# Performance work log

Measured on AMD Instinct MI355X. Metric: run time of the kernel, lower is better.

The kernel has to match this reference:

```python
import jax, jax.numpy as jnp
import numpy as np

N_NODES = 20000
N_EDGES = 320000
IN_C = 256
HID = 32
HEADS0 = 4  # n_heads[0]: both #modules in first layer and heads per module
OUT_C = 40
NEG_SLOPE = 0.2


def _segment_softmax(e, seg, n):
    # e: [E, H], softmax over edges grouped by destination node
    m = jax.ops.segment_max(e, seg, num_segments=n)
    m = jnp.where(jnp.isfinite(m), m, 0.0)  # nodes with no in-edges
    ex = jnp.exp(e - m[seg])
    s = jax.ops.segment_sum(ex, seg, num_segments=n)
    return ex / (s[seg] + 1e-16)


def _gat_conv(x, W, a_src, a_dst, bias, src, dst, n, concat):
    # PyG GATConv math (self-loops assumed already appended to src/dst)
    H, C = a_src.shape
    h = (x @ W).reshape(n, H, C)                      # [N, H, C]
    e_src = (h * a_src).sum(-1)                       # [N, H]
    e_dst = (h * a_dst).sum(-1)                       # [N, H]
    e = jax.nn.leaky_relu(e_src[src] + e_dst[dst], NEG_SLOPE)  # [E, H]
    alpha = _segment_softmax(e, dst, n)               # [E, H]
    out = jax.ops.segment_sum(h[src] * alpha[:, :, None], dst, num_segments=n)
    if concat:
        return out.reshape(n, H * C) + bias
    return out.mean(axis=1) + bias


def setup_inputs() -> dict:
    key = jax.random.key(0)
    ks = jax.random.split(key, 12)
    x = jax.random.normal(ks[0], (N_NODES, IN_C), dtype=jnp.float32)
    edge_index = jax.random.randint(ks[1], (2, N_EDGES), 0, N_NODES, dtype=jnp.int32)
    M = HEADS0  # number of first-layer modules
    W1 = jax.random.normal(ks[2], (M, IN_C, HEADS0 * HID), dtype=jnp.float32) * 0.1
    a_src1 = jax.random.normal(ks[3], (M, HEADS0, HID), dtype=jnp.float32) * 0.1
    a_dst1 = jax.random.normal(ks[4], (M, HEADS0, HID), dtype=jnp.float32) * 0.1
    b1 = jax.random.normal(ks[5], (M, HEADS0 * HID), dtype=jnp.float32) * 0.1
    cat_dim = M * HEADS0 * HID  # 512: actual width after torch.cat over modules
    W2 = jax.random.normal(ks[6], (cat_dim, OUT_C), dtype=jnp.float32) * 0.1
    a_src2 = jax.random.normal(ks[7], (1, OUT_C), dtype=jnp.float32) * 0.1
    a_dst2 = jax.random.normal(ks[8], (1, OUT_C), dtype=jnp.float32) * 0.1
    b2 = jax.random.normal(ks[9], (OUT_C,), dtype=jnp.float32) * 0.1
    return {"x": x, "edge_index": edge_index, "W1": W1, "a_src1": a_src1,
            "a_dst1": a_dst1, "b1": b1, "W2": W2, "a_src2": a_src2,
            "a_dst2": a_dst2, "b2": b2}


def reference(x, edge_index, W1, a_src1, a_dst1, b1, W2, a_src2, a_dst2, b2):
    n = x.shape[0]
    loops = jnp.arange(n, dtype=edge_index.dtype)  # PyG add_self_loops=True
    src = jnp.concatenate([edge_index[0], loops])
    dst = jnp.concatenate([edge_index[1], loops])
    # first layer: HEADS0 independent GATConv modules, outputs concatenated
    outs = jax.vmap(lambda W, a_s, a_d, b: _gat_conv(x, W, a_s, a_d, b, src, dst, n, True))(
        W1, a_src1, a_dst1, b1)                      # [M, N, HEADS0*HID]
    h = jnp.transpose(outs, (1, 0, 2)).reshape(n, -1)  # [N, 512]
    h = jax.nn.elu(h)  # dropout is a no-op in eval mode
    out = _gat_conv(h, W2, a_src2, a_dst2, b2, src, dst, n, False)  # [N, OUT_C]
    return jax.nn.log_softmax(out, axis=1)
```

## Files before the change

### kernel.cpp

```cpp
#include <hip/hip_runtime.h>
#include <cstdint>
#include <cstddef>

#define N_NODES 20000
#define N_EDGES 320000
#define E_TOT   340000
#define IN_C    256
#define HID     32
#define HEADS0  4
#define OUT_C   40
#define NEG_SLOPE 0.2f
#define CAT     512
#define MH      16
#define H2S     48

typedef unsigned short ushort_t;
typedef __attribute__((ext_vector_type(8))) short short8v;
typedef __attribute__((ext_vector_type(4))) float f32x4;
typedef __attribute__((ext_vector_type(8))) unsigned short ushort8v;

#define WAVE_FENCE() asm volatile("" ::: "memory")

__device__ inline float bf2f(unsigned short u) {
  union { unsigned int i; float f; } c; c.i = ((unsigned int)u) << 16; return c.f;
}
__device__ inline unsigned short f2bf(float f) {
  union { float f; unsigned int i; } c; c.f = f;
  unsigned int r = c.i + 0x7FFFu + ((c.i >> 16) & 1u);
  return (unsigned short)(r >> 16);
}


__global__ __launch_bounds__(256) void degree_k(const int* __restrict__ ei, int* __restrict__ deg) {
  int e = blockIdx.x * 256 + threadIdx.x;
  if (e >= E_TOT) return;
  int d = (e < N_EDGES) ? ei[N_EDGES + e] : (e - N_EDGES);
  atomicAdd(&deg[d], 1);
}

__global__ __launch_bounds__(1024) void scan_k(const int* __restrict__ deg, int* __restrict__ row_ptr) {
  const int C = 20;
  __shared__ int part[1024];
  int t = threadIdx.x;
  int b = t * C;
  int s = 0;
  for (int i = 0; i < C; i++) { int idx = b + i; if (idx < N_NODES) s += deg[idx]; }
  part[t] = s;
  __syncthreads();
  for (int off = 1; off < 1024; off <<= 1) {
    int v = part[t];
    int u = (t >= off) ? part[t - off] : 0;
    __syncthreads();
    part[t] = v + u;
    __syncthreads();
  }
  int run = (t > 0) ? part[t - 1] : 0;
  for (int i = 0; i < C; i++) {
    int idx = b + i;
    if (idx <= N_NODES) {
      row_ptr[idx] = run;
      if (idx < N_NODES) run += deg[idx];
    }
  }
}

__global__ __launch_bounds__(256) void scatter_score_k(const int* __restrict__ ei,
                                                       const int* __restrict__ row_ptr,
                                                       int* __restrict__ fill,
                                                       int* __restrict__ csr_src,
                                                       const float* __restrict__ es1,
                                                       const float* __restrict__ ed1,
                                                       ushort_t* __restrict__ exq) {
  int e = blockIdx.x * 256 + threadIdx.x;
  if (e >= E_TOT) return;
  int s, d;
  if (e < N_EDGES) { s = ei[e]; d = ei[N_EDGES + e]; }
  else             { s = e - N_EDGES; d = s; }
  int pos = row_ptr[d] + atomicAdd(&fill[d], 1);
  csr_src[pos] = s;

  const float4* sp = (const float4*)(es1 + (size_t)s * MH);
  const float4* dp = (const float4*)(ed1 + (size_t)d * MH);
  float4 a0 = sp[0], a1 = sp[1], a2 = sp[2], a3 = sp[3];
  float4 b0 = dp[0], b1 = dp[1], b2 = dp[2], b3 = dp[3];
  float v[16] = {a0.x + b0.x, a0.y + b0.y, a0.z + b0.z, a0.w + b0.w,
                 a1.x + b1.x, a1.y + b1.y, a1.z + b1.z, a1.w + b1.w,
                 a2.x + b2.x, a2.y + b2.y, a2.z + b2.z, a2.w + b2.w,
                 a3.x + b3.x, a3.y + b3.y, a3.z + b3.z, a3.w + b3.w};
  ushort8v o0, o1;
#pragma unroll
  for (int i = 0; i < 16; i++) {
    float ev = v[i];
    ev = (ev > 0.f) ? ev : ev * NEG_SLOPE;
    float ex = __expf(ev);
    if (i < 8) o0[i] = f2bf(ex); else o1[i - 8] = f2bf(ex);
  }
  *(ushort8v*)(exq + (size_t)pos * MH)     = o0;
  *(ushort8v*)(exq + (size_t)pos * MH + 8) = o1;
}

#define XB (N_NODES * IN_C / 4 / 256)

__global__ __launch_bounds__(256) void prep_k(const float* __restrict__ x,
                                              ushort_t* __restrict__ xhi,
                                              ushort_t* __restrict__ xlo,
                                              const float* __restrict__ W1,
                                              ushort_t* __restrict__ bhi,
                                              ushort_t* __restrict__ blo,
                                              const float* __restrict__ W2,
                                              ushort_t* __restrict__ b2hi,
                                              ushort_t* __restrict__ b2lo) {
  int blk = blockIdx.x;
  if (blk < XB) {
    int i = blk * 256 + threadIdx.x;
    float4 v = ((const float4*)x)[i];
    ushort_t hi[4], lo[4];
    float vv[4] = {v.x, v.y, v.z, v.w};
#pragma unroll
    for (int k = 0; k < 4; k++) {
      ushort_t h = f2bf(vv[k]);
      hi[k] = h;
      lo[k] = f2bf(vv[k] - bf2f(h));
    }
    ((ushort4*)xhi)[i] = make_ushort4(hi[0], hi[1], hi[2], hi[3]);
    ((ushort4*)xlo)[i] = make_ushort4(lo[0], lo[1], lo[2], lo[3]);
  } else if (blk < XB + 64) {
    int idx = (blk - XB) * 256 + threadIdx.x;
    int n16  = idx >> 9;
    int k32  = (idx >> 6) & 7;
    int lane = idx & 63;
    int cfull = n16 * 16 + (lane & 15);
    int m = cfull >> 7;
    int c = cfull & 127;
    int kbase = k32 * 32 + (lane >> 4) * 8;
#pragma unroll
    for (int b = 0; b < 8; b++) {
      float v = W1[((m << 8) + kbase + b) * 128 + c];
      ushort_t h = f2bf(v);
      bhi[(size_t)idx * 8 + b] = h;
      blo[(size_t)idx * 8 + b] = f2bf(v - bf2f(h));
    }
  } else {
    int idx = (blk - XB - 64) * 256 + threadIdx.x;
    int n16  = idx >> 10;
    int k32  = (idx >> 6) & 15;
    int lane = idx & 63;
    int n = n16 * 16 + (lane & 15);
    int kbase = k32 * 32 + (lane >> 4) * 8;
#pragma unroll
    for (int b = 0; b < 8; b++) {
      float v = (n < OUT_C) ? W2[(kbase + b) * OUT_C + n] : 0.f;
      ushort_t h = f2bf(v);
      b2hi[(size_t)idx * 8 + b] = h;
      b2lo[(size_t)idx * 8 + b] = f2bf(v - bf2f(h));
    }
  }
}

__global__ __launch_bounds__(256) void gemm1_mfma_k(const ushort_t* __restrict__ xhi,
                                                    const ushort_t* __restrict__ xlo,
                                                    const ushort_t* __restrict__ bhi,
                                                    const ushort_t* __restrict__ blo,
                                                    const float* __restrict__ a_src1,
                                                    const float* __restrict__ a_dst1,
                                                    ushort_t* __restrict__ h1b,
                                                    float* __restrict__ es1,
                                                    float* __restrict__ ed1) {
  int tid = threadIdx.x;
  int wave = tid >> 6, lane = tid & 63;
  int l15 = lane & 15, lhi = lane >> 4;
  int wrow = blockIdx.x * 64 + (wave & 1) * 32;
  int wcol = blockIdx.y * 128 + (wave >> 1) * 64;
  int n16base = wcol >> 4;

  f32x4 acc[2][4];
#pragma unroll
  for (int mf = 0; mf < 2; mf++)
#pragma unroll
    for (int nf = 0; nf < 4; nf++) acc[mf][nf] = (f32x4){0.f, 0.f, 0.f, 0.f};

  int arow[2];
#pragma unroll
  for (int mf = 0; mf < 2; mf++) {
    int r = wrow + mf * 16 + l15;
    arow[mf] = (r < N_NODES) ? r : (N_NODES - 1);
  }

  for (int ks = 0; ks < 8; ks++) {
    short8v ah[2], al[2];
#pragma unroll
    for (int mf = 0; mf < 2; mf++) {
      size_t off = (size_t)arow[mf] * IN_C + ks * 32 + lhi * 8;
      ah[mf] = *(const short8v*)(xhi + off);
      al[mf] = *(const short8v*)(xlo + off);
    }
    short8v bh[4], bl[4];
#pragma unroll
    for (int nf = 0; nf < 4; nf++) {
      size_t off = ((size_t)((n16base + nf) * 8 + ks) * 64 + lane) * 8;
      bh[nf] = *(const short8v*)(bhi + off);
      bl[nf] = *(const short8v*)(blo + off);
    }
#pragma unroll
    for (int mf = 0; mf < 2; mf++)
#pragma unroll
      for (int nf = 0; nf < 4; nf++) {
        acc[mf][nf] = __builtin_amdgcn_mfma_f32_16x16x32_bf16(ah[mf], bh[nf], acc[mf][nf], 0, 0, 0);
        acc[mf][nf] = __builtin_amdgcn_mfma_f32_16x16x32_bf16(ah[mf], bl[nf], acc[mf][nf], 0, 0, 0);
        acc[mf][nf] = __builtin_amdgcn_mfma_f32_16x16x32_bf16(al[mf], bh[nf], acc[mf][nf], 0, 0, 0);
      }
  }

#pragma unroll
  for (int mf = 0; mf < 2; mf++) {
    int rbase = wrow + mf * 16 + lhi * 4;
#pragma unroll
    for (int nf = 0; nf < 4; nf++) {
      int col = wcol + nf * 16 + l15;
#pragma unroll
      for (int r = 0; r < 4; r++) {
        int row = rbase + r;
        if (row < N_NODES)
          h1b[(size_t)row * CAT + col] = f2bf(acc[mf][nf][r]);
      }
    }
  }

  int mh0 = wcol >> 5;
  float as[4], ad[4];
#pragma unroll
  for (int nf = 0; nf < 4; nf++) {
    int aidx = (mh0 + (nf >> 1)) * HID + (nf & 1) * 16 + l15;
    as[nf] = a_src1[aidx];
    ad[nf] = a_dst1[aidx];
  }
#pragma unroll
  for (int mf = 0; mf < 2; mf++) {
#pragma unroll
    for (int r = 0; r < 4; r++) {
      int row = wrow + mf * 16 + lhi * 4 + r;
      float ps0 = acc[mf][0][r] * as[0] + acc[mf][1][r] * as[1];
      float ps1 = acc[mf][2][r] * as[2] + acc[mf][3][r] * as[3];
      float pd0 = acc[mf][0][r] * ad[0] + acc[mf][1][r] * ad[1];
      float pd1 = acc[mf][2][r] * ad[2] + acc[mf][3][r] * ad[3];
#pragma unroll
      for (int msk = 1; msk < 16; msk <<= 1) {
        ps0 += __shfl_xor(ps0, msk); ps1 += __shfl_xor(ps1, msk);
        pd0 += __shfl_xor(pd0, msk); pd1 += __shfl_xor(pd1, msk);
      }
      if (l15 == 0 && row < N_NODES) {
        es1[row * MH + mh0]     = ps0;
        es1[row * MH + mh0 + 1] = ps1;
        ed1[row * MH + mh0]     = pd0;
        ed1[row * MH + mh0 + 1] = pd1;
      }
    }
  }
}


__global__ __launch_bounds__(256) void agg1_k(const ushort_t* __restrict__ h1b,
                                              const ushort_t* __restrict__ exq,
                                              const int* __restrict__ row_ptr,
                                              const int* __restrict__ csr_src,
                                              const float* __restrict__ b1,
                                              ushort_t* __restrict__ hhi,
                                              ushort_t* __restrict__ hlo) {
  int w = threadIdx.x >> 6, lane = threadIdx.x & 63;
  int n = blockIdx.x * 4 + w;
  int beg = row_ptr[n];
  int deg = row_ptr[n + 1] - beg;
  int hh = lane >> 2;

  __shared__ float ex_buf[4][64][MH + 1];
  __shared__ int   src_buf[4][64];

  float s_part[MH];
#pragma unroll
  for (int i = 0; i < MH; i++) s_part[i] = 0.f;
  float acc[8];
#pragma unroll
  for (int j = 0; j < 8; j++) acc[j] = 0.f;

  for (int base = 0; base < deg; base += 64) {
    int cnt = min(64, deg - base);
    if (lane < cnt) {
      int p = beg + base + lane;
      src_buf[w][lane] = csr_src[p];
      ushort8v q0 = *(const ushort8v*)(exq + (size_t)p * MH);
      ushort8v q1 = *(const ushort8v*)(exq + (size_t)p * MH + 8);
#pragma unroll
      for (int i = 0; i < 8; i++) {
        float ex = bf2f(q0[i]);
        ex_buf[w][lane][i] = ex;
        s_part[i] += ex;
      }
#pragma unroll
      for (int i = 0; i < 8; i++) {
        float ex = bf2f(q1[i]);
        ex_buf[w][lane][8 + i] = ex;
        s_part[8 + i] += ex;
      }
    }
    WAVE_FENCE();
    int e = 0;
    for (; e + 3 < cnt; e += 4) {
      int s0 = src_buf[w][e + 0], s1 = src_buf[w][e + 1];
      int s2 = src_buf[w][e + 2], s3 = src_buf[w][e + 3];
      float x0 = ex_buf[w][e + 0][hh], x1 = ex_buf[w][e + 1][hh];
      float x2 = ex_buf[w][e + 2][hh], x3 = ex_buf[w][e + 3][hh];
      ushort8v v0 = *(const ushort8v*)(h1b + (size_t)s0 * CAT + lane * 8);
      ushort8v v1 = *(const ushort8v*)(h1b + (size_t)s1 * CAT + lane * 8);
      ushort8v v2 = *(const ushort8v*)(h1b + (size_t)s2 * CAT + lane * 8);
      ushort8v v3 = *(const ushort8v*)(h1b + (size_t)s3 * CAT + lane * 8);
#pragma unroll
      for (int j = 0; j < 8; j++) acc[j] += x0 * bf2f(v0[j]);
#pragma unroll
      for (int j = 0; j < 8; j++) acc[j] += x1 * bf2f(v1[j]);
#pragma unroll
      for (int j = 0; j < 8; j++) acc[j] += x2 * bf2f(v2[j]);
#pragma unroll
      for (int j = 0; j < 8; j++) acc[j] += x3 * bf2f(v3[j]);
    }
    for (; e < cnt; e++) {
      int s = src_buf[w][e];
      float xv = ex_buf[w][e][hh];
      ushort8v hv = *(const ushort8v*)(h1b + (size_t)s * CAT + lane * 8);
#pragma unroll
      for (int j = 0; j < 8; j++) acc[j] += xv * bf2f(hv[j]);
    }
    WAVE_FENCE();
  }

  float denom = 0.f;
#pragma unroll
  for (int i = 0; i < MH; i++) {
    float v = s_part[i];
    v += __shfl_xor(v, 1);  v += __shfl_xor(v, 2);  v += __shfl_xor(v, 4);
    v += __shfl_xor(v, 8);  v += __shfl_xor(v, 16); v += __shfl_xor(v, 32);
    if (hh == i) denom = v;
  }
  denom += 1e-16f;

  const float4* b1p = (const float4*)(b1 + lane * 8);
  float4 bq0 = b1p[0], bq1 = b1p[1];
  float bv8[8] = {bq0.x, bq0.y, bq0.z, bq0.w, bq1.x, bq1.y, bq1.z, bq1.w};

  ushort8v vhi, vlo;
#pragma unroll
  for (int j = 0; j < 8; j++) {
    float o = acc[j] / denom + bv8[j];
    float e = (o > 0.f) ? o : (__expf(o) - 1.f);
    ushort_t h = f2bf(e);
    vhi[j] = h;
    vlo[j] = f2bf(e - bf2f(h));
  }
  *(ushort8v*)(hhi + (size_t)n * CAT + lane * 8) = vhi;
  *(ushort8v*)(hlo + (size_t)n * CAT + lane * 8) = vlo;
}

__global__ __launch_bounds__(256) void gemm2_mfma_k(const ushort_t* __restrict__ hhi,
                                                    const ushort_t* __restrict__ hlo,
                                                    const ushort_t* __restrict__ b2hi,
                                                    const ushort_t* __restrict__ b2lo,
                                                    const float* __restrict__ a_src2,
                                                    const float* __restrict__ a_dst2,
                                                    ushort_t* __restrict__ h2b,
                                                    float* __restrict__ es2,
                                                    float* __restrict__ ed2) {
  int tid = threadIdx.x;
  int wave = tid >> 6, lane = tid & 63;
  int l15 = lane & 15, lhi = lane >> 4;
  int wrow = blockIdx.x * 64 + wave * 16;

  f32x4 acc[3];
#pragma unroll
  for (int nf = 0; nf < 3; nf++) acc[nf] = (f32x4){0.f, 0.f, 0.f, 0.f};

  int r0 = wrow + l15;
  int arow = (r0 < N_NODES) ? r0 : (N_NODES - 1);

  for (int ks = 0; ks < 16; ks++) {
    size_t aoff = (size_t)arow * CAT + ks * 32 + lhi * 8;
    short8v ah = *(const short8v*)(hhi + aoff);
    short8v al = *(const short8v*)(hlo + aoff);
#pragma unroll
    for (int nf = 0; nf < 3; nf++) {
      size_t boff = ((size_t)(nf * 16 + ks) * 64 + lane) * 8;
      short8v bh = *(const short8v*)(b2hi + boff);
      short8v bl = *(const short8v*)(b2lo + boff);
      acc[nf] = __builtin_amdgcn_mfma_f32_16x16x32_bf16(ah, bh, acc[nf], 0, 0, 0);
      acc[nf] = __builtin_amdgcn_mfma_f32_16x16x32_bf16(ah, bl, acc[nf], 0, 0, 0);
      acc[nf] = __builtin_amdgcn_mfma_f32_16x16x32_bf16(al, bh, acc[nf], 0, 0, 0);
    }
  }

  float av[3], bv[3];
#pragma unroll
  for (int nf = 0; nf < 3; nf++) {
    int col = nf * 16 + l15;
    av[nf] = (col < OUT_C) ? a_src2[col] : 0.f;
    bv[nf] = (col < OUT_C) ? a_dst2[col] : 0.f;
  }
#pragma unroll
  for (int r = 0; r < 4; r++) {
    int row = wrow + lhi * 4 + r;
    float ps = acc[0][r] * av[0] + acc[1][r] * av[1] + acc[2][r] * av[2];
    float pd = acc[0][r] * bv[0] + acc[1][r] * bv[1] + acc[2][r] * bv[2];
    ps += __shfl_xor(ps, 1); pd += __shfl_xor(pd, 1);
    ps += __shfl_xor(ps, 2); pd += __shfl_xor(pd, 2);
    ps += __shfl_xor(ps, 4); pd += __shfl_xor(pd, 4);
    ps += __shfl_xor(ps, 8); pd += __shfl_xor(pd, 8);
    if (row < N_NODES) {
#pragma unroll
      for (int nf = 0; nf < 3; nf++)
        h2b[(size_t)row * H2S + nf * 16 + l15] = f2bf(acc[nf][r]);
      if (l15 == 0) { es2[row] = ps; ed2[row] = pd; }
    }
  }
}

__global__ __launch_bounds__(256) void agg2_k(const ushort_t* __restrict__ h2b,
                                              const float* __restrict__ es2,
                                              const float* __restrict__ ed2,
                                              const int* __restrict__ row_ptr,
                                              const int* __restrict__ csr_src,
                                              const float* __restrict__ b2,
                                              float* __restrict__ out) {
  int w = threadIdx.x >> 6, lane = threadIdx.x & 63;
  int n = blockIdx.x * 4 + w;
  int beg = row_ptr[n];
  int deg = row_ptr[n + 1] - beg;
  float edn = ed2[n];

  __shared__ float exb[4][64];
  __shared__ int   srb[4][64];

  float acc = 0.f, ssum = 0.f;
  for (int base = 0; base < deg; base += 64) {
    int cnt = min(64, deg - base);
    if (lane < cnt) {
      int s = csr_src[beg + base + lane];
      srb[w][lane] = s;
      float ev = es2[s] + edn;
      ev = (ev > 0.f) ? ev : ev * NEG_SLOPE;
      float ex = __expf(ev);
      exb[w][lane] = ex;
      ssum += ex;
    }
    WAVE_FENCE();
    int e = 0;
    for (; e + 3 < cnt; e += 4) {
      int s0 = srb[w][e], s1 = srb[w][e + 1], s2 = srb[w][e + 2], s3 = srb[w][e + 3];
      float x0 = exb[w][e], x1 = exb[w][e + 1], x2 = exb[w][e + 2], x3 = exb[w][e + 3];
      if (lane < OUT_C) {
        float v0 = bf2f(h2b[(size_t)s0 * H2S + lane]);
        float v1 = bf2f(h2b[(size_t)s1 * H2S + lane]);
        float v2 = bf2f(h2b[(size_t)s2 * H2S + lane]);
        float v3 = bf2f(h2b[(size_t)s3 * H2S + lane]);
        acc += x0 * v0; acc += x1 * v1; acc += x2 * v2; acc += x3 * v3;
      }
    }
    for (; e < cnt; e++) {
      int s = srb[w][e];
      float xv = exb[w][e];
      if (lane < OUT_C) acc += xv * bf2f(h2b[(size_t)s * H2S + lane]);
    }
    WAVE_FENCE();
  }

  ssum += __shfl_xor(ssum, 1); ssum += __shfl_xor(ssum, 2); ssum += __shfl_xor(ssum, 4);
  ssum += __shfl_xor(ssum, 8); ssum += __shfl_xor(ssum, 16); ssum += __shfl_xor(ssum, 32);

  float val = (lane < OUT_C) ? (acc / (ssum + 1e-16f) + b2[lane]) : -INFINITY;

  float rmax = val;
#pragma unroll
  for (int o = 1; o < 64; o <<= 1) rmax = fmaxf(rmax, __shfl_xor(rmax, o));
  float ex = (lane < OUT_C) ? __expf(val - rmax) : 0.f;
  float sume = ex;
#pragma unroll
  for (int o = 1; o < 64; o <<= 1) sume += __shfl_xor(sume, o);
  if (lane < OUT_C) out[(size_t)n * OUT_C + lane] = val - rmax - __logf(sume);
}


extern "C" void kernel_launch(void* const* d_in, const int* in_sizes, int n_in,
                              void* d_out, int out_size, void* d_ws, size_t ws_size,
                              hipStream_t stream) {
  const float* x      = (const float*)d_in[0];
  const int*   ei     = (const int*)d_in[1];
  const float* W1     = (const float*)d_in[2];
  const float* a_src1 = (const float*)d_in[3];
  const float* a_dst1 = (const float*)d_in[4];
  const float* b1     = (const float*)d_in[5];
  const float* W2     = (const float*)d_in[6];
  const float* a_src2 = (const float*)d_in[7];
  const float* a_dst2 = (const float*)d_in[8];
  const float* b2     = (const float*)d_in[9];
  float* out = (float*)d_out;

  char* ws = (char*)d_ws;
  size_t off = 0;
  auto alloc = [&](size_t bytes) -> void* {
    void* p = ws + off;
    off += (bytes + 255) & ~(size_t)255;
    return p;
  };
  ushort_t* xhi  = (ushort_t*)alloc((size_t)N_NODES * IN_C * 2);
  ushort_t* xlo  = (ushort_t*)alloc((size_t)N_NODES * IN_C * 2);
  ushort_t* bhi  = (ushort_t*)alloc((size_t)32 * 8 * 64 * 8 * 2);
  ushort_t* blo  = (ushort_t*)alloc((size_t)32 * 8 * 64 * 8 * 2);
  ushort_t* b2hi = (ushort_t*)alloc((size_t)3 * 16 * 64 * 8 * 2);
  ushort_t* b2lo = (ushort_t*)alloc((size_t)3 * 16 * 64 * 8 * 2);
  ushort_t* h1b  = (ushort_t*)alloc((size_t)N_NODES * CAT * 2);
  ushort_t* hhi  = (ushort_t*)alloc((size_t)N_NODES * CAT * 2);
  ushort_t* hlo  = (ushort_t*)alloc((size_t)N_NODES * CAT * 2);
  float* es1     = (float*)alloc((size_t)N_NODES * MH * 4);
  float* ed1     = (float*)alloc((size_t)N_NODES * MH * 4);
  ushort_t* h2b  = (ushort_t*)alloc((size_t)N_NODES * H2S * 2);
  float* es2     = (float*)alloc((size_t)N_NODES * 4);
  float* ed2     = (float*)alloc((size_t)N_NODES * 4);
  int*   deg     = (int*)alloc((size_t)N_NODES * 4);
  int*   fill    = (int*)alloc((size_t)N_NODES * 4);
  int*   row_ptr = (int*)alloc((size_t)(N_NODES + 1) * 4);
  int*   csr_src = (int*)alloc((size_t)E_TOT * 4);
  ushort_t* exq  = xhi;

  hipMemsetAsync(deg, 0, ((size_t)N_NODES * 4 + 255 & ~(size_t)255) + (size_t)N_NODES * 4, stream);

  degree_k<<<(E_TOT + 255) / 256, 256, 0, stream>>>(ei, deg);
  scan_k<<<1, 1024, 0, stream>>>(deg, row_ptr);
  prep_k<<<XB + 64 + 12, 256, 0, stream>>>(x, xhi, xlo, W1, bhi, blo, W2, b2hi, b2lo);
  gemm1_mfma_k<<<dim3((N_NODES + 63) / 64, CAT / 128), 256, 0, stream>>>(
      xhi, xlo, bhi, blo, a_src1, a_dst1, h1b, es1, ed1);
  scatter_score_k<<<(E_TOT + 255) / 256, 256, 0, stream>>>(
      ei, row_ptr, fill, csr_src, es1, ed1, exq);
  agg1_k<<<N_NODES / 4, 256, 0, stream>>>(h1b, exq, row_ptr, csr_src, b1, hhi, hlo);
  gemm2_mfma_k<<<(N_NODES + 63) / 64, 256, 0, stream>>>(hhi, hlo, b2hi, b2lo, a_src2, a_dst2, h2b, es2, ed2);
  agg2_k<<<N_NODES / 4, 256, 0, stream>>>(h2b, es2, ed2, row_ptr, csr_src, b2, out);
}
```

Measured before the change: 207.8 us.

## Split x to bf16 hi/lo inside gemm1, fold degree count into prep, drop lo term in gemm2

```diff
diff --git a/kernel.cpp b/kernel.cpp
--- a/kernel.cpp
+++ b/kernel.cpp
@@ -30,12 +30,54 @@
   return (unsigned short)(r >> 16);
 }
 
-
-__global__ __launch_bounds__(256) void degree_k(const int* __restrict__ ei, int* __restrict__ deg) {
-  int e = blockIdx.x * 256 + threadIdx.x;
-  if (e >= E_TOT) return;
-  int d = (e < N_EDGES) ? ei[N_EDGES + e] : (e - N_EDGES);
-  atomicAdd(&deg[d], 1);
+#define DEGB ((E_TOT + 255) / 256)
+
+__global__ __launch_bounds__(256) void prep_k(const float* __restrict__ W1,
+                                              ushort_t* __restrict__ bhi,
+                                              ushort_t* __restrict__ blo,
+                                              const float* __restrict__ W2,
+                                              ushort_t* __restrict__ b2hi,
+                                              ushort_t* __restrict__ b2lo,
+                                              const int* __restrict__ ei,
+                                              int* __restrict__ deg) {
+  int blk = blockIdx.x;
+  if (blk < 64) {
+    int idx = blk * 256 + threadIdx.x;
+    int n16  = idx >> 9;
+    int k32  = (idx >> 6) & 7;
+    int lane = idx & 63;
+    int cfull = n16 * 16 + (lane & 15);
+    int m = cfull >> 7;
+    int c = cfull & 127;
+    int kbase = k32 * 32 + (lane >> 4) * 8;
+#pragma unroll
+    for (int b = 0; b < 8; b++) {
+      float v = W1[((m << 8) + kbase + b) * 128 + c];
+      ushort_t h = f2bf(v);
+      bhi[(size_t)idx * 8 + b] = h;
+      blo[(size_t)idx * 8 + b] = f2bf(v - bf2f(h));
+    }
+  } else if (blk < 76) {
+    int idx = (blk - 64) * 256 + threadIdx.x;
+    int n16  = idx >> 10;
+    int k32  = (idx >> 6) & 15;
+    int lane = idx & 63;
+    int n = n16 * 16 + (lane & 15);
+    int kbase = k32 * 32 + (lane >> 4) * 8;
+#pragma unroll
+    for (int b = 0; b < 8; b++) {
+      float v = (n < OUT_C) ? W2[(kbase + b) * OUT_C + n] : 0.f;
+      ushort_t h = f2bf(v);
+      b2hi[(size_t)idx * 8 + b] = h;
+      b2lo[(size_t)idx * 8 + b] = f2bf(v - bf2f(h));
+    }
+  } else {
+    int e = (blk - 76) * 256 + threadIdx.x;
+    if (e < E_TOT) {
+      int d = (e < N_EDGES) ? ei[N_EDGES + e] : (e - N_EDGES);
+      atomicAdd(&deg[d], 1);
+    }
+  }
 }
 
 __global__ __launch_bounds__(1024) void scan_k(const int* __restrict__ deg, int* __restrict__ row_ptr) {
@@ -99,66 +141,7 @@
   *(ushort8v*)(exq + (size_t)pos * MH + 8) = o1;
 }
 
-#define XB (N_NODES * IN_C / 4 / 256)
-
-__global__ __launch_bounds__(256) void prep_k(const float* __restrict__ x,
-                                              ushort_t* __restrict__ xhi,
-                                              ushort_t* __restrict__ xlo,
-                                              const float* __restrict__ W1,
-                                              ushort_t* __restrict__ bhi,
-                                              ushort_t* __restrict__ blo,
-                                              const float* __restrict__ W2,
-                                              ushort_t* __restrict__ b2hi,
-                                              ushort_t* __restrict__ b2lo) {
-  int blk = blockIdx.x;
-  if (blk < XB) {
-    int i = blk * 256 + threadIdx.x;
-    float4 v = ((const float4*)x)[i];
-    ushort_t hi[4], lo[4];
-    float vv[4] = {v.x, v.y, v.z, v.w};
-#pragma unroll
-    for (int k = 0; k < 4; k++) {
-      ushort_t h = f2bf(vv[k]);
-      hi[k] = h;
-      lo[k] = f2bf(vv[k] - bf2f(h));
-    }
-    ((ushort4*)xhi)[i] = make_ushort4(hi[0], hi[1], hi[2], hi[3]);
-    ((ushort4*)xlo)[i] = make_ushort4(lo[0], lo[1], lo[2], lo[3]);
-  } else if (blk < XB + 64) {
-    int idx = (blk - XB) * 256 + threadIdx.x;
-    int n16  = idx >> 9;
-    int k32  = (idx >> 6) & 7;
-    int lane = idx & 63;
-    int cfull = n16 * 16 + (lane & 15);
-    int m = cfull >> 7;
-    int c = cfull & 127;
-    int kbase = k32 * 32 + (lane >> 4) * 8;
-#pragma unroll
-    for (int b = 0; b < 8; b++) {
-      float v = W1[((m << 8) + kbase + b) * 128 + c];
-      ushort_t h = f2bf(v);
-      bhi[(size_t)idx * 8 + b] = h;
-      blo[(size_t)idx * 8 + b] = f2bf(v - bf2f(h));
-    }
-  } else {
-    int idx = (blk - XB - 64) * 256 + threadIdx.x;
-    int n16  = idx >> 10;
-    int k32  = (idx >> 6) & 15;
-    int lane = idx & 63;
-    int n = n16 * 16 + (lane & 15);
-    int kbase = k32 * 32 + (lane >> 4) * 8;
-#pragma unroll
-    for (int b = 0; b < 8; b++) {
-      float v = (n < OUT_C) ? W2[(kbase + b) * OUT_C + n] : 0.f;
-      ushort_t h = f2bf(v);
-      b2hi[(size_t)idx * 8 + b] = h;
-      b2lo[(size_t)idx * 8 + b] = f2bf(v - bf2f(h));
-    }
-  }
-}
-
-__global__ __launch_bounds__(256) void gemm1_mfma_k(const ushort_t* __restrict__ xhi,
-                                                    const ushort_t* __restrict__ xlo,
+__global__ __launch_bounds__(256) void gemm1_mfma_k(const float* __restrict__ x,
                                                     const ushort_t* __restrict__ bhi,
                                                     const ushort_t* __restrict__ blo,
                                                     const float* __restrict__ a_src1,
@@ -190,9 +173,15 @@
     short8v ah[2], al[2];
 #pragma unroll
     for (int mf = 0; mf < 2; mf++) {
-      size_t off = (size_t)arow[mf] * IN_C + ks * 32 + lhi * 8;
-      ah[mf] = *(const short8v*)(xhi + off);
-      al[mf] = *(const short8v*)(xlo + off);
+      const float4* xp = (const float4*)(x + (size_t)arow[mf] * IN_C + ks * 32 + lhi * 8);
+      float4 f0 = xp[0], f1 = xp[1];
+      float av8[8] = {f0.x, f0.y, f0.z, f0.w, f1.x, f1.y, f1.z, f1.w};
+#pragma unroll
+      for (int j = 0; j < 8; j++) {
+        ushort_t h = f2bf(av8[j]);
+        ah[mf][j] = (short)h;
+        al[mf][j] = (short)f2bf(av8[j] - bf2f(h));
+      }
     }
     short8v bh[4], bl[4];
 #pragma unroll
@@ -264,8 +253,7 @@
                                               const int* __restrict__ row_ptr,
                                               const int* __restrict__ csr_src,
                                               const float* __restrict__ b1,
-                                              ushort_t* __restrict__ hhi,
-                                              ushort_t* __restrict__ hlo) {
+                                              ushort_t* __restrict__ h1e) {
   int w = threadIdx.x >> 6, lane = threadIdx.x & 63;
   int n = blockIdx.x * 4 + w;
   int beg = row_ptr[n];
@@ -346,21 +334,17 @@
   float4 bq0 = b1p[0], bq1 = b1p[1];
   float bv8[8] = {bq0.x, bq0.y, bq0.z, bq0.w, bq1.x, bq1.y, bq1.z, bq1.w};
 
-  ushort8v vhi, vlo;
+  ushort8v vhi;
 #pragma unroll
   for (int j = 0; j < 8; j++) {
     float o = acc[j] / denom + bv8[j];
     float e = (o > 0.f) ? o : (__expf(o) - 1.f);
-    ushort_t h = f2bf(e);
-    vhi[j] = h;
-    vlo[j] = f2bf(e - bf2f(h));
-  }
-  *(ushort8v*)(hhi + (size_t)n * CAT + lane * 8) = vhi;
-  *(ushort8v*)(hlo + (size_t)n * CAT + lane * 8) = vlo;
-}
-
-__global__ __launch_bounds__(256) void gemm2_mfma_k(const ushort_t* __restrict__ hhi,
-                                                    const ushort_t* __restrict__ hlo,
+    vhi[j] = f2bf(e);
+  }
+  *(ushort8v*)(h1e + (size_t)n * CAT + lane * 8) = vhi;
+}
+
+__global__ __launch_bounds__(256) void gemm2_mfma_k(const ushort_t* __restrict__ h1e,
                                                     const ushort_t* __restrict__ b2hi,
                                                     const ushort_t* __restrict__ b2lo,
                                                     const float* __restrict__ a_src2,
@@ -382,8 +366,7 @@
 
   for (int ks = 0; ks < 16; ks++) {
     size_t aoff = (size_t)arow * CAT + ks * 32 + lhi * 8;
-    short8v ah = *(const short8v*)(hhi + aoff);
-    short8v al = *(const short8v*)(hlo + aoff);
+    short8v ah = *(const short8v*)(h1e + aoff);
 #pragma unroll
     for (int nf = 0; nf < 3; nf++) {
       size_t boff = ((size_t)(nf * 16 + ks) * 64 + lane) * 8;
@@ -391,7 +374,6 @@
       short8v bl = *(const short8v*)(b2lo + boff);
       acc[nf] = __builtin_amdgcn_mfma_f32_16x16x32_bf16(ah, bh, acc[nf], 0, 0, 0);
       acc[nf] = __builtin_amdgcn_mfma_f32_16x16x32_bf16(ah, bl, acc[nf], 0, 0, 0);
-      acc[nf] = __builtin_amdgcn_mfma_f32_16x16x32_bf16(al, bh, acc[nf], 0, 0, 0);
     }
   }
 
@@ -507,15 +489,13 @@
     off += (bytes + 255) & ~(size_t)255;
     return p;
   };
-  ushort_t* xhi  = (ushort_t*)alloc((size_t)N_NODES * IN_C * 2);
-  ushort_t* xlo  = (ushort_t*)alloc((size_t)N_NODES * IN_C * 2);
   ushort_t* bhi  = (ushort_t*)alloc((size_t)32 * 8 * 64 * 8 * 2);
   ushort_t* blo  = (ushort_t*)alloc((size_t)32 * 8 * 64 * 8 * 2);
   ushort_t* b2hi = (ushort_t*)alloc((size_t)3 * 16 * 64 * 8 * 2);
   ushort_t* b2lo = (ushort_t*)alloc((size_t)3 * 16 * 64 * 8 * 2);
   ushort_t* h1b  = (ushort_t*)alloc((size_t)N_NODES * CAT * 2);
-  ushort_t* hhi  = (ushort_t*)alloc((size_t)N_NODES * CAT * 2);
-  ushort_t* hlo  = (ushort_t*)alloc((size_t)N_NODES * CAT * 2);
+  ushort_t* h1e  = (ushort_t*)alloc((size_t)N_NODES * CAT * 2);
+  ushort_t* exq  = (ushort_t*)alloc((size_t)E_TOT * MH * 2);
   float* es1     = (float*)alloc((size_t)N_NODES * MH * 4);
   float* ed1     = (float*)alloc((size_t)N_NODES * MH * 4);
   ushort_t* h2b  = (ushort_t*)alloc((size_t)N_NODES * H2S * 2);
@@ -525,18 +505,16 @@
   int*   fill    = (int*)alloc((size_t)N_NODES * 4);
   int*   row_ptr = (int*)alloc((size_t)(N_NODES + 1) * 4);
   int*   csr_src = (int*)alloc((size_t)E_TOT * 4);
-  ushort_t* exq  = xhi;
-
-  hipMemsetAsync(deg, 0, ((size_t)N_NODES * 4 + 255 & ~(size_t)255) + (size_t)N_NODES * 4, stream);
-
-  degree_k<<<(E_TOT + 255) / 256, 256, 0, stream>>>(ei, deg);
+
+  hipMemsetAsync(deg, 0, (((size_t)N_NODES * 4 + 255) & ~(size_t)255) + (size_t)N_NODES * 4, stream);
+
+  prep_k<<<64 + 12 + DEGB, 256, 0, stream>>>(W1, bhi, blo, W2, b2hi, b2lo, ei, deg);
   scan_k<<<1, 1024, 0, stream>>>(deg, row_ptr);
-  prep_k<<<XB + 64 + 12, 256, 0, stream>>>(x, xhi, xlo, W1, bhi, blo, W2, b2hi, b2lo);
   gemm1_mfma_k<<<dim3((N_NODES + 63) / 64, CAT / 128), 256, 0, stream>>>(
-      xhi, xlo, bhi, blo, a_src1, a_dst1, h1b, es1, ed1);
+      x, bhi, blo, a_src1, a_dst1, h1b, es1, ed1);
   scatter_score_k<<<(E_TOT + 255) / 256, 256, 0, stream>>>(
       ei, row_ptr, fill, csr_src, es1, ed1, exq);
-  agg1_k<<<N_NODES / 4, 256, 0, stream>>>(h1b, exq, row_ptr, csr_src, b1, hhi, hlo);
-  gemm2_mfma_k<<<(N_NODES + 63) / 64, 256, 0, stream>>>(hhi, hlo, b2hi, b2lo, a_src2, a_dst2, h2b, es2, ed2);
+  agg1_k<<<N_NODES / 4, 256, 0, stream>>>(h1b, exq, row_ptr, csr_src, b1, h1e);
+  gemm2_mfma_k<<<(N_NODES + 63) / 64, 256, 0, stream>>>(h1e, b2hi, b2lo, a_src2, a_dst2, h2b, es2, ed2);
   agg2_k<<<N_NODES / 4, 256, 0, stream>>>(h2b, es2, ed2, row_ptr, csr_src, b2, out);
 }
```

New measurement: 193.1 us. 1.08x faster.
